# Optimization experiments

Measured on AMD Instinct MI355X. Metric: run time of the kernel, lower is better.

The kernel has to match this reference:

```python
import jax, jax.numpy as jnp
import numpy as np

B, S, D, H = 64, 2048, 64, 128  # batch, seq_len, input_dim, rnn_hidden_dim


def setup_inputs() -> dict:
    key = jax.random.key(0)
    k = jax.random.split(key, 6)
    x = jax.random.normal(k[0], (B, S, D), dtype=jnp.float32)
    # LSTM params, keras gate order: i, f, g(candidate), o
    Wx = jax.random.normal(k[1], (D, 4 * H), dtype=jnp.float32) / np.sqrt(D)
    Wh = jax.random.normal(k[2], (H, 4 * H), dtype=jnp.float32) / np.sqrt(H)
    b = jnp.zeros((4 * H,), dtype=jnp.float32).at[H:2 * H].set(1.0)  # unit_forget_bias
    # Dense(1, sigmoid) head
    Wd = jax.random.normal(k[3], (H, 1), dtype=jnp.float32) / np.sqrt(H)
    bd = jnp.zeros((1,), dtype=jnp.float32)
    return {"x": x, "Wx": Wx, "Wh": Wh, "b": b, "Wd": Wd, "bd": bd}


def _lstm_seq(x, Wx, Wh, b):
    H_ = Wh.shape[0]
    # precompute input projections for all timesteps: [B,S,4H]
    xz = jnp.einsum('bsd,dg->bsg', x, Wx) + b

    def step(carry, xz_t):
        h, c = carry
        z = xz_t + h @ Wh  # [B,4H]
        i = jax.nn.sigmoid(z[:, :H_])
        f = jax.nn.sigmoid(z[:, H_:2 * H_])
        g = jnp.tanh(z[:, 2 * H_:3 * H_])
        o = jax.nn.sigmoid(z[:, 3 * H_:])
        c = f * c + i * g
        h = o * jnp.tanh(c)
        return (h, c), h

    h0 = jnp.zeros((x.shape[0], H_), dtype=x.dtype)
    c0 = jnp.zeros((x.shape[0], H_), dtype=x.dtype)
    _, hs = jax.lax.scan(step, (h0, c0), jnp.swapaxes(xz, 0, 1))  # hs: [S,B,H]
    return jnp.swapaxes(hs, 0, 1)  # [B,S,H]


def reference(x, Wx, Wh, b, Wd, bd):
    h = _lstm_seq(x, Wx, Wh, b)                 # [B,S,H]
    return jax.nn.sigmoid(h @ Wd + bd)          # [B,S,1]
```

## Files before the change

### kernel.cpp

```cpp
#include <hip/hip_runtime.h>

#define B_ 64
#define S_ 2048
#define D_ 64
#define H_ 128
#define G_ 512
#define CH 16

typedef float f32x4 __attribute__((ext_vector_type(4)));
typedef short bf16x8 __attribute__((ext_vector_type(8)));

#define MFMA16(a, b, c) __builtin_amdgcn_mfma_f32_16x16x32_bf16((a), (b), (c), 0, 0, 0)
#define RCPF(x) __builtin_amdgcn_rcpf(x)
#define LOG2E 1.442695041f

#if __has_builtin(__builtin_amdgcn_exp2f)
#define EXP2(x) __builtin_amdgcn_exp2f(x)
#else
#define EXP2(x) exp2f(x)
#endif

#define STEP_SYNC() do {                                  \
    asm volatile("s_waitcnt lgkmcnt(0)" ::: "memory");    \
    __builtin_amdgcn_s_barrier();                         \
    asm volatile("" ::: "memory");                        \
} while (0)

__device__ __forceinline__ short f2bf(float f) {
    unsigned u = __builtin_bit_cast(unsigned, f);
    return (short)((u + 0x7FFFu + ((u >> 16) & 1u)) >> 16);
}
__device__ __forceinline__ float bflo(unsigned u) { return __builtin_bit_cast(float, u << 16); }
__device__ __forceinline__ float bfhi(unsigned u) { return __builtin_bit_cast(float, u & 0xFFFF0000u); }
__device__ __forceinline__ float sigm_f(float x) { return RCPF(1.0f + EXP2(x * -LOG2E)); }
__device__ __forceinline__ float tanh_f(float x) {
    return __builtin_fmaf(2.0f, RCPF(1.0f + EXP2(x * (-2.0f * LOG2E))), -1.0f);
}

__launch_bounds__(512, 2)
__global__ void lstm_fused(const float* __restrict__ x, const float* __restrict__ Wx,
                           const float* __restrict__ Wh, const float* __restrict__ bias,
                           const float* __restrict__ Wd, const float* __restrict__ bd,
                           float* __restrict__ out) {
    const int tid = threadIdx.x;
    const int lane = tid & 63;
    const int wid = tid >> 6;
    const int l15 = lane & 15;
    const int l4 = lane >> 4;
    const int bb = blockIdx.x;

    __shared__ alignas(16) short hist[CH][H_];
    __shared__ alignas(16) short xbf[CH][72];
    __shared__ alignas(16) float xzc[CH][G_];

    ((unsigned*)hist)[tid] = 0u;
    ((unsigned*)hist)[tid + 512] = 0u;

    const int col0 = wid * 16 + l15;

    bf16x8 bh[4][4];
#pragma unroll
    for (int ct = 0; ct < 4; ++ct) {
        const int col = ct * H_ + col0;
#pragma unroll
        for (int kt = 0; kt < 4; ++kt) {
            bf16x8 v;
#pragma unroll
            for (int e = 0; e < 8; ++e)
                v[e] = f2bf(Wh[(kt * 32 + l4 * 8 + e) * G_ + col]);
            bh[ct][kt] = v;
        }
    }
    bf16x8 bx[4][2];
#pragma unroll
    for (int ct = 0; ct < 4; ++ct) {
        const int col = ct * H_ + col0;
#pragma unroll
        for (int kt = 0; kt < 2; ++kt) {
            bf16x8 v;
#pragma unroll
            for (int e = 0; e < 8; ++e)
                v[e] = f2bf(Wx[(kt * 32 + l4 * 8 + e) * G_ + col]);
            bx[ct][kt] = v;
        }
    }

    float bvr[4];
#pragma unroll
    for (int ct = 0; ct < 4; ++ct) bvr[ct] = bias[ct * H_ + col0];
    const float wd0 = Wd[lane * 2 + 0];
    const float wd1 = Wd[lane * 2 + 1];
    const float bdv = bd[0];
    float c_reg = 0.0f;

    const float* xb = x + (size_t)bb * S_ * D_;
    float* ob = out + (size_t)bb * S_;

    float xp0 = xb[tid * 2 + 0];
    float xp1 = xb[tid * 2 + 1];

    f32x4 acc0 = {0.f, 0.f, 0.f, 0.f}, acc1 = acc0, acc2 = acc0, acc3 = acc0;

    for (int tc = 0; tc < S_; tc += CH) {
        xbf[tid >> 5][(tid & 31) * 2 + 0] = f2bf(xp0);
        xbf[tid >> 5][(tid & 31) * 2 + 1] = f2bf(xp1);
        __syncthreads();
        if (tc + CH < S_) {
            xp0 = xb[(tc + CH) * D_ + tid * 2 + 0];
            xp1 = xb[(tc + CH) * D_ + tid * 2 + 1];
        }
#pragma unroll
        for (int ct = 0; ct < 4; ++ct) {
            f32x4 cacc = {bvr[ct], bvr[ct], bvr[ct], bvr[ct]};
#pragma unroll
            for (int kt = 0; kt < 2; ++kt) {
                const bf16x8 a = *reinterpret_cast<const bf16x8*>(&xbf[l15][kt * 32 + l4 * 8]);
                cacc = MFMA16(a, bx[ct][kt], cacc);
            }
#pragma unroll
            for (int r = 0; r < 4; ++r)
                xzc[l4 * 4 + r][col0 * 4 + ct] = cacc[r];
        }
        if (tc > 0) {
#pragma unroll
            for (int s = 0; s < 2; ++s) {
                const int row = wid * 2 + s;
                const unsigned hp = *reinterpret_cast<const unsigned*>(&hist[row][lane * 2]);
                float p = bflo(hp) * wd0 + bfhi(hp) * wd1;
                p += __shfl_xor(p, 1);  p += __shfl_xor(p, 2);  p += __shfl_xor(p, 4);
                p += __shfl_xor(p, 8);  p += __shfl_xor(p, 16); p += __shfl_xor(p, 32);
                if (lane == 0) ob[tc - CH + row] = sigm_f(p + bdv);
            }
        }
        __syncthreads();

#pragma unroll
        for (int tm = 0; tm < CH; ++tm) {
            const int prev = (tm + CH - 1) & (CH - 1);
            const short* hsrc = hist[prev];
            const bf16x8 a0 = *reinterpret_cast<const bf16x8*>(&hsrc[ 0 + l4 * 8]);
            const bf16x8 a1 = *reinterpret_cast<const bf16x8*>(&hsrc[32 + l4 * 8]);
            const bf16x8 a2 = *reinterpret_cast<const bf16x8*>(&hsrc[64 + l4 * 8]);
            const bf16x8 a3 = *reinterpret_cast<const bf16x8*>(&hsrc[96 + l4 * 8]);
            const f32x4 xzq = *reinterpret_cast<const f32x4*>(&xzc[tm][col0 * 4]);

            acc0[0] = xzq[0];  acc1[0] = xzq[1];  acc2[0] = xzq[2];  acc3[0] = xzq[3];

            acc0 = MFMA16(a0, bh[0][0], acc0);
            acc1 = MFMA16(a0, bh[1][0], acc1);
            acc2 = MFMA16(a0, bh[2][0], acc2);
            acc3 = MFMA16(a0, bh[3][0], acc3);
            acc0 = MFMA16(a1, bh[0][1], acc0);
            acc1 = MFMA16(a1, bh[1][1], acc1);
            acc2 = MFMA16(a1, bh[2][1], acc2);
            acc3 = MFMA16(a1, bh[3][1], acc3);
            acc0 = MFMA16(a2, bh[0][2], acc0);
            acc1 = MFMA16(a2, bh[1][2], acc1);
            acc2 = MFMA16(a2, bh[2][2], acc2);
            acc3 = MFMA16(a2, bh[3][2], acc3);
            acc0 = MFMA16(a3, bh[0][3], acc0);
            acc1 = MFMA16(a3, bh[1][3], acc1);
            acc2 = MFMA16(a3, bh[2][3], acc2);
            acc3 = MFMA16(a3, bh[3][3], acc3);

            const float iv = sigm_f(acc0[0]);
            const float fv = sigm_f(acc1[0]);
            const float gv = tanh_f(acc2[0]);
            const float ov = sigm_f(acc3[0]);

            c_reg = __builtin_fmaf(fv, c_reg, iv * gv);
            const float hv = ov * tanh_f(c_reg);

            if (lane < 16) hist[tm][col0] = f2bf(hv);
            STEP_SYNC();
        }
    }

#pragma unroll
    for (int s = 0; s < 2; ++s) {
        const int row = wid * 2 + s;
        const unsigned hp = *reinterpret_cast<const unsigned*>(&hist[row][lane * 2]);
        float p = bflo(hp) * wd0 + bfhi(hp) * wd1;
        p += __shfl_xor(p, 1);  p += __shfl_xor(p, 2);  p += __shfl_xor(p, 4);
        p += __shfl_xor(p, 8);  p += __shfl_xor(p, 16); p += __shfl_xor(p, 32);
        if (lane == 0) ob[S_ - CH + row] = sigm_f(p + bdv);
    }
}

extern "C" void kernel_launch(void* const* d_in, const int* in_sizes, int n_in,
                              void* d_out, int out_size, void* d_ws, size_t ws_size,
                              hipStream_t stream) {
    const float* x  = (const float*)d_in[0];
    const float* Wx = (const float*)d_in[1];
    const float* Wh = (const float*)d_in[2];
    const float* b  = (const float*)d_in[3];
    const float* Wd = (const float*)d_in[4];
    const float* bd = (const float*)d_in[5];
    float* out = (float*)d_out;

    lstm_fused<<<B_, 512, 0, stream>>>(x, Wx, Wh, b, Wd, bd, out);
}
```

Measured before the change: 955.5 us.

## Double-buffer h/xz chunks and interleave input projection into recurrent steps

Double-buffers the hidden-state history and the precomputed input projections, so the next chunk's x load, bf16 conversion, input-projection MFMAs and the previous chunk's dense-head output are spread across individual timesteps of the current chunk. This removes the two per-chunk __syncthreads phases that stalled the serial recurrence. It also folds the -log2e (and -2log2e for the candidate gate) scaling into Wx, Wh and bias, which drops the multiplies in the gate activations. The trade-off is more LDS use, more conditional code inside the unrolled step loop and higher register pressure, and the scaling is applied before bf16 rounding.

```diff
diff --git a/kernel.cpp b/kernel.cpp
--- a/kernel.cpp
+++ b/kernel.cpp
@@ -6,6 +6,7 @@
 #define H_ 128
 #define G_ 512
 #define CH 16
+#define NCHUNK (S_ / CH)
 
 typedef float f32x4 __attribute__((ext_vector_type(4)));
 typedef short bf16x8 __attribute__((ext_vector_type(8)));
@@ -33,9 +34,6 @@
 __device__ __forceinline__ float bflo(unsigned u) { return __builtin_bit_cast(float, u << 16); }
 __device__ __forceinline__ float bfhi(unsigned u) { return __builtin_bit_cast(float, u & 0xFFFF0000u); }
 __device__ __forceinline__ float sigm_f(float x) { return RCPF(1.0f + EXP2(x * -LOG2E)); }
-__device__ __forceinline__ float tanh_f(float x) {
-    return __builtin_fmaf(2.0f, RCPF(1.0f + EXP2(x * (-2.0f * LOG2E))), -1.0f);
-}
 
 __launch_bounds__(512, 2)
 __global__ void lstm_fused(const float* __restrict__ x, const float* __restrict__ Wx,
@@ -49,45 +47,50 @@
     const int l4 = lane >> 4;
     const int bb = blockIdx.x;
 
-    __shared__ alignas(16) short hist[CH][H_];
+    __shared__ alignas(16) short hbuf[2][CH][H_];
     __shared__ alignas(16) short xbf[CH][72];
-    __shared__ alignas(16) float xzc[CH][G_];
-
-    ((unsigned*)hist)[tid] = 0u;
-    ((unsigned*)hist)[tid + 512] = 0u;
+    __shared__ alignas(16) float xzc[2][CH][G_];
+
+    {
+        unsigned* hz = (unsigned*)hbuf;
+        hz[tid] = 0u; hz[tid + 512] = 0u; hz[tid + 1024] = 0u; hz[tid + 1536] = 0u;
+    }
 
     const int col0 = wid * 16 + l15;
 
     bf16x8 bh[4][4];
 #pragma unroll
     for (int ct = 0; ct < 4; ++ct) {
+        const float msc = (ct == 2) ? (-2.0f * LOG2E) : (-LOG2E);
         const int col = ct * H_ + col0;
 #pragma unroll
         for (int kt = 0; kt < 4; ++kt) {
             bf16x8 v;
 #pragma unroll
             for (int e = 0; e < 8; ++e)
-                v[e] = f2bf(Wh[(kt * 32 + l4 * 8 + e) * G_ + col]);
+                v[e] = f2bf(Wh[(kt * 32 + l4 * 8 + e) * G_ + col] * msc);
             bh[ct][kt] = v;
         }
     }
     bf16x8 bx[4][2];
 #pragma unroll
     for (int ct = 0; ct < 4; ++ct) {
+        const float msc = (ct == 2) ? (-2.0f * LOG2E) : (-LOG2E);
         const int col = ct * H_ + col0;
 #pragma unroll
         for (int kt = 0; kt < 2; ++kt) {
             bf16x8 v;
 #pragma unroll
             for (int e = 0; e < 8; ++e)
-                v[e] = f2bf(Wx[(kt * 32 + l4 * 8 + e) * G_ + col]);
+                v[e] = f2bf(Wx[(kt * 32 + l4 * 8 + e) * G_ + col] * msc);
             bx[ct][kt] = v;
         }
     }
 
     float bvr[4];
 #pragma unroll
-    for (int ct = 0; ct < 4; ++ct) bvr[ct] = bias[ct * H_ + col0];
+    for (int ct = 0; ct < 4; ++ct)
+        bvr[ct] = bias[ct * H_ + col0] * ((ct == 2) ? (-2.0f * LOG2E) : (-LOG2E));
     const float wd0 = Wd[lane * 2 + 0];
     const float wd1 = Wd[lane * 2 + 1];
     const float bdv = bd[0];
@@ -96,53 +99,47 @@
     const float* xb = x + (size_t)bb * S_ * D_;
     float* ob = out + (size_t)bb * S_;
 
-    float xp0 = xb[tid * 2 + 0];
-    float xp1 = xb[tid * 2 + 1];
-
-    f32x4 acc0 = {0.f, 0.f, 0.f, 0.f}, acc1 = acc0, acc2 = acc0, acc3 = acc0;
-
-    for (int tc = 0; tc < S_; tc += CH) {
-        xbf[tid >> 5][(tid & 31) * 2 + 0] = f2bf(xp0);
-        xbf[tid >> 5][(tid & 31) * 2 + 1] = f2bf(xp1);
+    float xp0, xp1;
+
+    {
+        const float a0v = xb[tid * 2 + 0];
+        const float a1v = xb[tid * 2 + 1];
+        const unsigned pk = ((unsigned)(unsigned short)f2bf(a0v)) |
+                            (((unsigned)(unsigned short)f2bf(a1v)) << 16);
+        *reinterpret_cast<unsigned*>(&xbf[tid >> 5][(tid & 31) * 2]) = pk;
         __syncthreads();
-        if (tc + CH < S_) {
-            xp0 = xb[(tc + CH) * D_ + tid * 2 + 0];
-            xp1 = xb[(tc + CH) * D_ + tid * 2 + 1];
-        }
+        xp0 = xb[CH * D_ + tid * 2 + 0];
+        xp1 = xb[CH * D_ + tid * 2 + 1];
 #pragma unroll
         for (int ct = 0; ct < 4; ++ct) {
-            f32x4 cacc = {bvr[ct], bvr[ct], bvr[ct], bvr[ct]};
+            f32x4 cc = {bvr[ct], bvr[ct], bvr[ct], bvr[ct]};
 #pragma unroll
             for (int kt = 0; kt < 2; ++kt) {
                 const bf16x8 a = *reinterpret_cast<const bf16x8*>(&xbf[l15][kt * 32 + l4 * 8]);
-                cacc = MFMA16(a, bx[ct][kt], cacc);
+                cc = MFMA16(a, bx[ct][kt], cc);
             }
 #pragma unroll
             for (int r = 0; r < 4; ++r)
-                xzc[l4 * 4 + r][col0 * 4 + ct] = cacc[r];
-        }
-        if (tc > 0) {
-#pragma unroll
-            for (int s = 0; s < 2; ++s) {
-                const int row = wid * 2 + s;
-                const unsigned hp = *reinterpret_cast<const unsigned*>(&hist[row][lane * 2]);
-                float p = bflo(hp) * wd0 + bfhi(hp) * wd1;
-                p += __shfl_xor(p, 1);  p += __shfl_xor(p, 2);  p += __shfl_xor(p, 4);
-                p += __shfl_xor(p, 8);  p += __shfl_xor(p, 16); p += __shfl_xor(p, 32);
-                if (lane == 0) ob[tc - CH + row] = sigm_f(p + bdv);
-            }
+                xzc[0][l4 * 4 + r][col0 * 4 + ct] = cc[r];
         }
         __syncthreads();
+    }
+
+    f32x4 acc0 = {0.f, 0.f, 0.f, 0.f}, acc1 = acc0, acc2 = acc0, acc3 = acc0;
+    bf16x8 gf0, gf1;
+
+    for (int k = 0; k < NCHUNK; ++k) {
+        const int cur = k & 1, prv = cur ^ 1;
+        const bool notlast = (k < NCHUNK - 1);
 
 #pragma unroll
         for (int tm = 0; tm < CH; ++tm) {
-            const int prev = (tm + CH - 1) & (CH - 1);
-            const short* hsrc = hist[prev];
+            const short* hsrc = (tm == 0) ? hbuf[prv][CH - 1] : hbuf[cur][tm - 1];
             const bf16x8 a0 = *reinterpret_cast<const bf16x8*>(&hsrc[ 0 + l4 * 8]);
             const bf16x8 a1 = *reinterpret_cast<const bf16x8*>(&hsrc[32 + l4 * 8]);
             const bf16x8 a2 = *reinterpret_cast<const bf16x8*>(&hsrc[64 + l4 * 8]);
             const bf16x8 a3 = *reinterpret_cast<const bf16x8*>(&hsrc[96 + l4 * 8]);
-            const f32x4 xzq = *reinterpret_cast<const f32x4*>(&xzc[tm][col0 * 4]);
+            const f32x4 xzq = *reinterpret_cast<const f32x4*>(&xzc[cur][tm][col0 * 4]);
 
             acc0[0] = xzq[0];  acc1[0] = xzq[1];  acc2[0] = xzq[2];  acc3[0] = xzq[3];
 
@@ -163,15 +160,50 @@
             acc2 = MFMA16(a3, bh[2][3], acc2);
             acc3 = MFMA16(a3, bh[3][3], acc3);
 
-            const float iv = sigm_f(acc0[0]);
-            const float fv = sigm_f(acc1[0]);
-            const float gv = tanh_f(acc2[0]);
-            const float ov = sigm_f(acc3[0]);
+            const float iv = RCPF(1.0f + EXP2(acc0[0]));
+            const float fv = RCPF(1.0f + EXP2(acc1[0]));
+            const float gv = __builtin_fmaf(2.0f, RCPF(1.0f + EXP2(acc2[0])), -1.0f);
+            const float ov = RCPF(1.0f + EXP2(acc3[0]));
 
             c_reg = __builtin_fmaf(fv, c_reg, iv * gv);
-            const float hv = ov * tanh_f(c_reg);
-
-            if (lane < 16) hist[tm][col0] = f2bf(hv);
+            const float th = __builtin_fmaf(
+                2.0f, RCPF(1.0f + EXP2(c_reg * (-2.0f * LOG2E))), -1.0f);
+            const float hv = ov * th;
+
+            if (lane < 16) hbuf[cur][tm][col0] = f2bf(hv);
+
+            if (tm == 0 && notlast) {
+                const unsigned pk = ((unsigned)(unsigned short)f2bf(xp0)) |
+                                    (((unsigned)(unsigned short)f2bf(xp1)) << 16);
+                *reinterpret_cast<unsigned*>(&xbf[tid >> 5][(tid & 31) * 2]) = pk;
+                if (k < NCHUNK - 2) {
+                    xp0 = xb[(k + 2) * CH * D_ + tid * 2 + 0];
+                    xp1 = xb[(k + 2) * CH * D_ + tid * 2 + 1];
+                }
+            }
+            if (tm == 1 && notlast)
+                gf0 = *reinterpret_cast<const bf16x8*>(&xbf[l15][ 0 + l4 * 8]);
+            if (tm == 3 && notlast)
+                gf1 = *reinterpret_cast<const bf16x8*>(&xbf[l15][32 + l4 * 8]);
+            if ((tm == 4 || tm == 6 || tm == 8 || tm == 10) && notlast) {
+                const int ct = (tm - 4) >> 1;
+                f32x4 cc = {bvr[ct], bvr[ct], bvr[ct], bvr[ct]};
+                cc = MFMA16(gf0, bx[ct][0], cc);
+                cc = MFMA16(gf1, bx[ct][1], cc);
+#pragma unroll
+                for (int r = 0; r < 4; ++r)
+                    xzc[prv][l4 * 4 + r][col0 * 4 + ct] = cc[r];
+            }
+            if ((tm == 5 || tm == 13) && k > 0) {
+                const int row = wid * 2 + (tm == 13 ? 1 : 0);
+                const unsigned hp =
+                    *reinterpret_cast<const unsigned*>(&hbuf[prv][row][lane * 2]);
+                float p = bflo(hp) * wd0 + bfhi(hp) * wd1;
+                p += __shfl_xor(p, 1);  p += __shfl_xor(p, 2);  p += __shfl_xor(p, 4);
+                p += __shfl_xor(p, 8);  p += __shfl_xor(p, 16); p += __shfl_xor(p, 32);
+                if (lane == 0) ob[(k - 1) * CH + row] = sigm_f(p + bdv);
+            }
+
             STEP_SYNC();
         }
     }
@@ -179,7 +211,7 @@
 #pragma unroll
     for (int s = 0; s < 2; ++s) {
         const int row = wid * 2 + s;
-        const unsigned hp = *reinterpret_cast<const unsigned*>(&hist[row][lane * 2]);
+        const unsigned hp = *reinterpret_cast<const unsigned*>(&hbuf[1][row][lane * 2]);
         float p = bflo(hp) * wd0 + bfhi(hp) * wd1;
         p += __shfl_xor(p, 1);  p += __shfl_xor(p, 2);  p += __shfl_xor(p, 4);
         p += __shfl_xor(p, 8);  p += __shfl_xor(p, 16); p += __shfl_xor(p, 32);
```

Result: no change. 954.4 us (-0.1%).

## Replace recurrent MFMA with per-lane fp16 dot2 matvec and gate shuffles

Applied to the files above, without the earlier changes.

Each lane now owns one gate column and holds that column of Wh in registers as 64 packed fp16 pairs. It computes the recurrent matvec with v_dot2 instructions on a broadcast LDS read of h, instead of sixteen 16x16x32 MFMAs where only row 0 of the output is useful. The -log2e scale for the activations is folded into Wh, Wx and the bias, so sigmoid and tanh share one exp2/rcp form. The four gates are exchanged with xor shuffles. The hidden state is stored as fp16 instead of bf16. This aims to remove wasted MFMA work and latency on the serial critical path, at the cost of 64 extra weight registers per lane, dependent dot2 chains, and fp16 range and precision risk.

```diff
diff --git a/kernel.cpp b/kernel.cpp
--- a/kernel.cpp
+++ b/kernel.cpp
@@ -9,6 +9,8 @@
 
 typedef float f32x4 __attribute__((ext_vector_type(4)));
 typedef short bf16x8 __attribute__((ext_vector_type(8)));
+typedef short short2v __attribute__((ext_vector_type(2)));
+typedef _Float16 half2v __attribute__((ext_vector_type(2)));
 
 #define MFMA16(a, b, c) __builtin_amdgcn_mfma_f32_16x16x32_bf16((a), (b), (c), 0, 0, 0)
 #define RCPF(x) __builtin_amdgcn_rcpf(x)
@@ -20,6 +22,15 @@
 #define EXP2(x) exp2f(x)
 #endif
 
+#if __has_builtin(__builtin_amdgcn_fdot2)
+#define DOT2(a, b, c) __builtin_amdgcn_fdot2((a), (b), (c), false)
+#else
+__device__ __forceinline__ float DOT2(half2v a, half2v b, float c) {
+    return __builtin_fmaf((float)a[1], (float)b[1],
+           __builtin_fmaf((float)a[0], (float)b[0], c));
+}
+#endif
+
 #define STEP_SYNC() do {                                  \
     asm volatile("s_waitcnt lgkmcnt(0)" ::: "memory");    \
     __builtin_amdgcn_s_barrier();                         \
@@ -30,12 +41,13 @@
     unsigned u = __builtin_bit_cast(unsigned, f);
     return (short)((u + 0x7FFFu + ((u >> 16) & 1u)) >> 16);
 }
-__device__ __forceinline__ float bflo(unsigned u) { return __builtin_bit_cast(float, u << 16); }
-__device__ __forceinline__ float bfhi(unsigned u) { return __builtin_bit_cast(float, u & 0xFFFF0000u); }
+__device__ __forceinline__ short f2h(float f) {
+    return __builtin_bit_cast(short, (_Float16)f);
+}
+__device__ __forceinline__ float h2f(short s) {
+    return (float)__builtin_bit_cast(_Float16, s);
+}
 __device__ __forceinline__ float sigm_f(float x) { return RCPF(1.0f + EXP2(x * -LOG2E)); }
-__device__ __forceinline__ float tanh_f(float x) {
-    return __builtin_fmaf(2.0f, RCPF(1.0f + EXP2(x * (-2.0f * LOG2E))), -1.0f);
-}
 
 __launch_bounds__(512, 2)
 __global__ void lstm_fused(const float* __restrict__ x, const float* __restrict__ Wx,
@@ -49,6 +61,10 @@
     const int l4 = lane >> 4;
     const int bb = blockIdx.x;
 
+    const int q = lane & 3;
+    const int u = wid * 16 + (lane >> 2);
+    const int col = q * H_ + u;
+
     __shared__ alignas(16) short hist[CH][H_];
     __shared__ alignas(16) short xbf[CH][72];
     __shared__ alignas(16) float xzc[CH][G_];
@@ -56,38 +72,39 @@
     ((unsigned*)hist)[tid] = 0u;
     ((unsigned*)hist)[tid + 512] = 0u;
 
-    const int col0 = wid * 16 + l15;
-
-    bf16x8 bh[4][4];
+    const float msc = (q == 2) ? (-2.0f * LOG2E) : (-LOG2E);
+    const float a_c = (q == 2) ? 2.0f : 1.0f;
+    const float b_c = (q == 2) ? -1.0f : 0.0f;
+
+    half2v wh[64];
+#pragma unroll
+    for (int p = 0; p < 64; ++p) {
+        half2v v;
+        v[0] = (_Float16)(Wh[(2 * p + 0) * G_ + col] * msc);
+        v[1] = (_Float16)(Wh[(2 * p + 1) * G_ + col] * msc);
+        wh[p] = v;
+    }
+
+    bf16x8 bx[4][2];
 #pragma unroll
     for (int ct = 0; ct < 4; ++ct) {
-        const int col = ct * H_ + col0;
-#pragma unroll
-        for (int kt = 0; kt < 4; ++kt) {
-            bf16x8 v;
-#pragma unroll
-            for (int e = 0; e < 8; ++e)
-                v[e] = f2bf(Wh[(kt * 32 + l4 * 8 + e) * G_ + col]);
-            bh[ct][kt] = v;
-        }
-    }
-    bf16x8 bx[4][2];
-#pragma unroll
-    for (int ct = 0; ct < 4; ++ct) {
-        const int col = ct * H_ + col0;
+        const float ms = (ct == 2) ? (-2.0f * LOG2E) : (-LOG2E);
+        const int colm = ct * H_ + wid * 16 + l15;
 #pragma unroll
         for (int kt = 0; kt < 2; ++kt) {
             bf16x8 v;
 #pragma unroll
             for (int e = 0; e < 8; ++e)
-                v[e] = f2bf(Wx[(kt * 32 + l4 * 8 + e) * G_ + col]);
+                v[e] = f2bf(Wx[(kt * 32 + l4 * 8 + e) * G_ + colm] * ms);
             bx[ct][kt] = v;
         }
     }
-
     float bvr[4];
 #pragma unroll
-    for (int ct = 0; ct < 4; ++ct) bvr[ct] = bias[ct * H_ + col0];
+    for (int ct = 0; ct < 4; ++ct)
+        bvr[ct] = bias[ct * H_ + wid * 16 + l15] *
+                  ((ct == 2) ? (-2.0f * LOG2E) : (-LOG2E));
+
     const float wd0 = Wd[lane * 2 + 0];
     const float wd1 = Wd[lane * 2 + 1];
     const float bdv = bd[0];
@@ -99,7 +116,8 @@
     float xp0 = xb[tid * 2 + 0];
     float xp1 = xb[tid * 2 + 1];
 
-    f32x4 acc0 = {0.f, 0.f, 0.f, 0.f}, acc1 = acc0, acc2 = acc0, acc3 = acc0;
+    const bool sb0 = (q & 1) != 0;
+    const bool sb1 = (q & 2) != 0;
 
     for (int tc = 0; tc < S_; tc += CH) {
         xbf[tid >> 5][(tid & 31) * 2 + 0] = f2bf(xp0);
@@ -111,22 +129,22 @@
         }
 #pragma unroll
         for (int ct = 0; ct < 4; ++ct) {
-            f32x4 cacc = {bvr[ct], bvr[ct], bvr[ct], bvr[ct]};
+            f32x4 cc = {bvr[ct], bvr[ct], bvr[ct], bvr[ct]};
 #pragma unroll
             for (int kt = 0; kt < 2; ++kt) {
                 const bf16x8 a = *reinterpret_cast<const bf16x8*>(&xbf[l15][kt * 32 + l4 * 8]);
-                cacc = MFMA16(a, bx[ct][kt], cacc);
+                cc = MFMA16(a, bx[ct][kt], cc);
             }
 #pragma unroll
             for (int r = 0; r < 4; ++r)
-                xzc[l4 * 4 + r][col0 * 4 + ct] = cacc[r];
+                xzc[l4 * 4 + r][(wid * 16 + l15) * 4 + ct] = cc[r];
         }
         if (tc > 0) {
 #pragma unroll
             for (int s = 0; s < 2; ++s) {
                 const int row = wid * 2 + s;
-                const unsigned hp = *reinterpret_cast<const unsigned*>(&hist[row][lane * 2]);
-                float p = bflo(hp) * wd0 + bfhi(hp) * wd1;
+                const short2v hp = *reinterpret_cast<const short2v*>(&hist[row][lane * 2]);
+                float p = h2f(hp[0]) * wd0 + h2f(hp[1]) * wd1;
                 p += __shfl_xor(p, 1);  p += __shfl_xor(p, 2);  p += __shfl_xor(p, 4);
                 p += __shfl_xor(p, 8);  p += __shfl_xor(p, 16); p += __shfl_xor(p, 32);
                 if (lane == 0) ob[tc - CH + row] = sigm_f(p + bdv);
@@ -138,40 +156,37 @@
         for (int tm = 0; tm < CH; ++tm) {
             const int prev = (tm + CH - 1) & (CH - 1);
             const short* hsrc = hist[prev];
-            const bf16x8 a0 = *reinterpret_cast<const bf16x8*>(&hsrc[ 0 + l4 * 8]);
-            const bf16x8 a1 = *reinterpret_cast<const bf16x8*>(&hsrc[32 + l4 * 8]);
-            const bf16x8 a2 = *reinterpret_cast<const bf16x8*>(&hsrc[64 + l4 * 8]);
-            const bf16x8 a3 = *reinterpret_cast<const bf16x8*>(&hsrc[96 + l4 * 8]);
-            const f32x4 xzq = *reinterpret_cast<const f32x4*>(&xzc[tm][col0 * 4]);
-
-            acc0[0] = xzq[0];  acc1[0] = xzq[1];  acc2[0] = xzq[2];  acc3[0] = xzq[3];
-
-            acc0 = MFMA16(a0, bh[0][0], acc0);
-            acc1 = MFMA16(a0, bh[1][0], acc1);
-            acc2 = MFMA16(a0, bh[2][0], acc2);
-            acc3 = MFMA16(a0, bh[3][0], acc3);
-            acc0 = MFMA16(a1, bh[0][1], acc0);
-            acc1 = MFMA16(a1, bh[1][1], acc1);
-            acc2 = MFMA16(a1, bh[2][1], acc2);
-            acc3 = MFMA16(a1, bh[3][1], acc3);
-            acc0 = MFMA16(a2, bh[0][2], acc0);
-            acc1 = MFMA16(a2, bh[1][2], acc1);
-            acc2 = MFMA16(a2, bh[2][2], acc2);
-            acc3 = MFMA16(a2, bh[3][2], acc3);
-            acc0 = MFMA16(a3, bh[0][3], acc0);
-            acc1 = MFMA16(a3, bh[1][3], acc1);
-            acc2 = MFMA16(a3, bh[2][3], acc2);
-            acc3 = MFMA16(a3, bh[3][3], acc3);
-
-            const float iv = sigm_f(acc0[0]);
-            const float fv = sigm_f(acc1[0]);
-            const float gv = tanh_f(acc2[0]);
-            const float ov = sigm_f(acc3[0]);
-
-            c_reg = __builtin_fmaf(fv, c_reg, iv * gv);
-            const float hv = ov * tanh_f(c_reg);
-
-            if (lane < 16) hist[tm][col0] = f2bf(hv);
+
+            float za = xzc[tm][u * 4 + q], zb = 0.0f, zc2 = 0.0f, zd = 0.0f;
+#pragma unroll
+            for (int j = 0; j < 16; ++j) {
+                const bf16x8 hr = *reinterpret_cast<const bf16x8*>(&hsrc[j * 8]);
+                const short2v s0 = {hr[0], hr[1]};
+                const short2v s1 = {hr[2], hr[3]};
+                const short2v s2 = {hr[4], hr[5]};
+                const short2v s3 = {hr[6], hr[7]};
+                za  = DOT2(__builtin_bit_cast(half2v, s0), wh[j * 4 + 0], za);
+                zb  = DOT2(__builtin_bit_cast(half2v, s1), wh[j * 4 + 1], zb);
+                zc2 = DOT2(__builtin_bit_cast(half2v, s2), wh[j * 4 + 2], zc2);
+                zd  = DOT2(__builtin_bit_cast(half2v, s3), wh[j * 4 + 3], zd);
+            }
+            const float z = (za + zb) + (zc2 + zd);
+
+            const float t = __builtin_fmaf(a_c, RCPF(1.0f + EXP2(z)), b_c);
+
+            const float t1 = __shfl_xor(t, 1);
+            const float t2 = __shfl_xor(t, 2);
+            const float t3 = __shfl_xor(t, 3);
+            const float ig = sb0 ? (t1 * t3) : (t * t2);
+            const float fv = sb0 ? (sb1 ? t2 : t) : (sb1 ? t3 : t1);
+            const float ov = sb0 ? (sb1 ? t : t2) : (sb1 ? t1 : t3);
+
+            c_reg = __builtin_fmaf(fv, c_reg, ig);
+            const float th = __builtin_fmaf(
+                2.0f, RCPF(1.0f + EXP2(c_reg * (-2.0f * LOG2E))), -1.0f);
+            const float hv = ov * th;
+
+            if (q == 0) hist[tm][u] = f2h(hv);
             STEP_SYNC();
         }
     }
@@ -179,8 +194,8 @@
 #pragma unroll
     for (int s = 0; s < 2; ++s) {
         const int row = wid * 2 + s;
-        const unsigned hp = *reinterpret_cast<const unsigned*>(&hist[row][lane * 2]);
-        float p = bflo(hp) * wd0 + bfhi(hp) * wd1;
+        const short2v hp = *reinterpret_cast<const short2v*>(&hist[row][lane * 2]);
+        float p = h2f(hp[0]) * wd0 + h2f(hp[1]) * wd1;
         p += __shfl_xor(p, 1);  p += __shfl_xor(p, 2);  p += __shfl_xor(p, 4);
         p += __shfl_xor(p, 8);  p += __shfl_xor(p, 16); p += __shfl_xor(p, 32);
         if (lane == 0) ob[S_ - CH + row] = sigm_f(p + bdv);
```

Measured after the change: 1.298 ms. 1.36x slower.

## Halve LSTM block to 4 waves with two hidden tiles per wave, prescaled gates

Applied to the files above, without the earlier changes.

Cuts the block from 8 to 4 waves, so each wave computes 32 hidden units (8 accumulator tiles) per timestep. This halves the number of waves meeting at each per-step barrier. The input weights move from registers into an LDS transposed copy to make room for the doubled Wh register footprint. The weights and bias are prescaled by -log2e (or -2log2e for the candidate gate) so the gate activations skip a multiply. The cost is a longer serial MFMA chain per wave each step, plus LDS reads of Wx in the chunk projection.

```diff
diff --git a/kernel.cpp b/kernel.cpp
--- a/kernel.cpp
+++ b/kernel.cpp
@@ -6,6 +6,7 @@
 #define H_ 128
 #define G_ 512
 #define CH 16
+#define T_ 256
 
 typedef float f32x4 __attribute__((ext_vector_type(4)));
 typedef short bf16x8 __attribute__((ext_vector_type(8)));
@@ -33,11 +34,8 @@
 __device__ __forceinline__ float bflo(unsigned u) { return __builtin_bit_cast(float, u << 16); }
 __device__ __forceinline__ float bfhi(unsigned u) { return __builtin_bit_cast(float, u & 0xFFFF0000u); }
 __device__ __forceinline__ float sigm_f(float x) { return RCPF(1.0f + EXP2(x * -LOG2E)); }
-__device__ __forceinline__ float tanh_f(float x) {
-    return __builtin_fmaf(2.0f, RCPF(1.0f + EXP2(x * (-2.0f * LOG2E))), -1.0f);
-}
-
-__launch_bounds__(512, 2)
+
+__launch_bounds__(256, 1)
 __global__ void lstm_fused(const float* __restrict__ x, const float* __restrict__ Wx,
                            const float* __restrict__ Wh, const float* __restrict__ bias,
                            const float* __restrict__ Wd, const float* __restrict__ bd,
@@ -49,82 +47,94 @@
     const int l4 = lane >> 4;
     const int bb = blockIdx.x;
 
+    __shared__ alignas(16) short wxt[G_][72];
+    __shared__ alignas(16) float xzc[CH][G_];
     __shared__ alignas(16) short hist[CH][H_];
     __shared__ alignas(16) short xbf[CH][72];
-    __shared__ alignas(16) float xzc[CH][G_];
-
-    ((unsigned*)hist)[tid] = 0u;
-    ((unsigned*)hist)[tid + 512] = 0u;
-
-    const int col0 = wid * 16 + l15;
-
-    bf16x8 bh[4][4];
-#pragma unroll
-    for (int ct = 0; ct < 4; ++ct) {
-        const int col = ct * H_ + col0;
-#pragma unroll
-        for (int kt = 0; kt < 4; ++kt) {
-            bf16x8 v;
-#pragma unroll
-            for (int e = 0; e < 8; ++e)
-                v[e] = f2bf(Wh[(kt * 32 + l4 * 8 + e) * G_ + col]);
-            bh[ct][kt] = v;
-        }
-    }
-    bf16x8 bx[4][2];
-#pragma unroll
-    for (int ct = 0; ct < 4; ++ct) {
-        const int col = ct * H_ + col0;
-#pragma unroll
-        for (int kt = 0; kt < 2; ++kt) {
-            bf16x8 v;
-#pragma unroll
-            for (int e = 0; e < 8; ++e)
-                v[e] = f2bf(Wx[(kt * 32 + l4 * 8 + e) * G_ + col]);
-            bx[ct][kt] = v;
-        }
-    }
-
-    float bvr[4];
-#pragma unroll
-    for (int ct = 0; ct < 4; ++ct) bvr[ct] = bias[ct * H_ + col0];
+
+    {
+        unsigned* hz = (unsigned*)hist;
+        hz[tid] = 0u; hz[tid + 256] = 0u; hz[tid + 512] = 0u; hz[tid + 768] = 0u;
+    }
+    for (int i = tid; i < G_ * D_; i += T_) {
+        const int colx = i & (G_ - 1);
+        const int row = i >> 9;
+        const float ms = ((colx >> 7) == 2) ? (-2.0f * LOG2E) : (-LOG2E);
+        wxt[colx][row] = f2bf(Wx[i] * ms);
+    }
+
+    bf16x8 bh[8][4];
+    float bvr[8];
+#pragma unroll
+    for (int hh = 0; hh < 2; ++hh) {
+#pragma unroll
+        for (int g = 0; g < 4; ++g) {
+            const float msc = (g == 2) ? (-2.0f * LOG2E) : (-LOG2E);
+            const int col = g * H_ + wid * 32 + hh * 16 + l15;
+            bvr[hh * 4 + g] = bias[col] * msc;
+#pragma unroll
+            for (int kt = 0; kt < 4; ++kt) {
+                bf16x8 v;
+#pragma unroll
+                for (int e = 0; e < 8; ++e)
+                    v[e] = f2bf(Wh[(kt * 32 + l4 * 8 + e) * G_ + col] * msc);
+                bh[hh * 4 + g][kt] = v;
+            }
+        }
+    }
+
     const float wd0 = Wd[lane * 2 + 0];
     const float wd1 = Wd[lane * 2 + 1];
     const float bdv = bd[0];
-    float c_reg = 0.0f;
+    float cA = 0.0f, cB = 0.0f;
 
     const float* xb = x + (size_t)bb * S_ * D_;
     float* ob = out + (size_t)bb * S_;
 
-    float xp0 = xb[tid * 2 + 0];
-    float xp1 = xb[tid * 2 + 1];
-
-    f32x4 acc0 = {0.f, 0.f, 0.f, 0.f}, acc1 = acc0, acc2 = acc0, acc3 = acc0;
+    float xp0 = xb[tid * 4 + 0], xp1 = xb[tid * 4 + 1];
+    float xp2 = xb[tid * 4 + 2], xp3 = xb[tid * 4 + 3];
+
+    f32x4 acc[8];
+#pragma unroll
+    for (int j = 0; j < 8; ++j) acc[j] = (f32x4){0.f, 0.f, 0.f, 0.f};
 
     for (int tc = 0; tc < S_; tc += CH) {
-        xbf[tid >> 5][(tid & 31) * 2 + 0] = f2bf(xp0);
-        xbf[tid >> 5][(tid & 31) * 2 + 1] = f2bf(xp1);
+        {
+            short* xr = &xbf[tid >> 4][(tid & 15) * 4];
+            xr[0] = f2bf(xp0); xr[1] = f2bf(xp1); xr[2] = f2bf(xp2); xr[3] = f2bf(xp3);
+        }
         __syncthreads();
         if (tc + CH < S_) {
-            xp0 = xb[(tc + CH) * D_ + tid * 2 + 0];
-            xp1 = xb[(tc + CH) * D_ + tid * 2 + 1];
-        }
-#pragma unroll
-        for (int ct = 0; ct < 4; ++ct) {
-            f32x4 cacc = {bvr[ct], bvr[ct], bvr[ct], bvr[ct]};
-#pragma unroll
-            for (int kt = 0; kt < 2; ++kt) {
-                const bf16x8 a = *reinterpret_cast<const bf16x8*>(&xbf[l15][kt * 32 + l4 * 8]);
-                cacc = MFMA16(a, bx[ct][kt], cacc);
+            xp0 = xb[(tc + CH) * D_ + tid * 4 + 0];
+            xp1 = xb[(tc + CH) * D_ + tid * 4 + 1];
+            xp2 = xb[(tc + CH) * D_ + tid * 4 + 2];
+            xp3 = xb[(tc + CH) * D_ + tid * 4 + 3];
+        }
+#pragma unroll
+        for (int hh = 0; hh < 2; ++hh) {
+#pragma unroll
+            for (int g = 0; g < 4; ++g) {
+                const int col = g * H_ + wid * 32 + hh * 16 + l15;
+                const float bv = bvr[hh * 4 + g];
+                f32x4 cc = {bv, bv, bv, bv};
+#pragma unroll
+                for (int kt = 0; kt < 2; ++kt) {
+                    const bf16x8 a = *reinterpret_cast<const bf16x8*>(
+                        &xbf[l15][kt * 32 + l4 * 8]);
+                    const bf16x8 b = *reinterpret_cast<const bf16x8*>(
+                        &wxt[col][kt * 32 + l4 * 8]);
+                    cc = MFMA16(a, b, cc);
+                }
+                const int unit = wid * 32 + hh * 16 + l15;
+#pragma unroll
+                for (int r = 0; r < 4; ++r)
+                    xzc[l4 * 4 + r][unit * 4 + g] = cc[r];
             }
-#pragma unroll
-            for (int r = 0; r < 4; ++r)
-                xzc[l4 * 4 + r][col0 * 4 + ct] = cacc[r];
         }
         if (tc > 0) {
 #pragma unroll
-            for (int s = 0; s < 2; ++s) {
-                const int row = wid * 2 + s;
+            for (int s = 0; s < 4; ++s) {
+                const int row = wid * 4 + s;
                 const unsigned hp = *reinterpret_cast<const unsigned*>(&hist[row][lane * 2]);
                 float p = bflo(hp) * wd0 + bfhi(hp) * wd1;
                 p += __shfl_xor(p, 1);  p += __shfl_xor(p, 2);  p += __shfl_xor(p, 4);
@@ -142,43 +152,51 @@
             const bf16x8 a1 = *reinterpret_cast<const bf16x8*>(&hsrc[32 + l4 * 8]);
             const bf16x8 a2 = *reinterpret_cast<const bf16x8*>(&hsrc[64 + l4 * 8]);
             const bf16x8 a3 = *reinterpret_cast<const bf16x8*>(&hsrc[96 + l4 * 8]);
-            const f32x4 xzq = *reinterpret_cast<const f32x4*>(&xzc[tm][col0 * 4]);
-
-            acc0[0] = xzq[0];  acc1[0] = xzq[1];  acc2[0] = xzq[2];  acc3[0] = xzq[3];
-
-            acc0 = MFMA16(a0, bh[0][0], acc0);
-            acc1 = MFMA16(a0, bh[1][0], acc1);
-            acc2 = MFMA16(a0, bh[2][0], acc2);
-            acc3 = MFMA16(a0, bh[3][0], acc3);
-            acc0 = MFMA16(a1, bh[0][1], acc0);
-            acc1 = MFMA16(a1, bh[1][1], acc1);
-            acc2 = MFMA16(a1, bh[2][1], acc2);
-            acc3 = MFMA16(a1, bh[3][1], acc3);
-            acc0 = MFMA16(a2, bh[0][2], acc0);
-            acc1 = MFMA16(a2, bh[1][2], acc1);
-            acc2 = MFMA16(a2, bh[2][2], acc2);
-            acc3 = MFMA16(a2, bh[3][2], acc3);
-            acc0 = MFMA16(a3, bh[0][3], acc0);
-            acc1 = MFMA16(a3, bh[1][3], acc1);
-            acc2 = MFMA16(a3, bh[2][3], acc2);
-            acc3 = MFMA16(a3, bh[3][3], acc3);
-
-            const float iv = sigm_f(acc0[0]);
-            const float fv = sigm_f(acc1[0]);
-            const float gv = tanh_f(acc2[0]);
-            const float ov = sigm_f(acc3[0]);
-
-            c_reg = __builtin_fmaf(fv, c_reg, iv * gv);
-            const float hv = ov * tanh_f(c_reg);
-
-            if (lane < 16) hist[tm][col0] = f2bf(hv);
+            const int uA = wid * 32 + l15;
+            const f32x4 xzA = *reinterpret_cast<const f32x4*>(&xzc[tm][uA * 4]);
+            const f32x4 xzB = *reinterpret_cast<const f32x4*>(&xzc[tm][(uA + 16) * 4]);
+
+            acc[0][0] = xzA[0];  acc[1][0] = xzA[1];
+            acc[2][0] = xzA[2];  acc[3][0] = xzA[3];
+            acc[4][0] = xzB[0];  acc[5][0] = xzB[1];
+            acc[6][0] = xzB[2];  acc[7][0] = xzB[3];
+
+#pragma unroll
+            for (int j = 0; j < 8; ++j) acc[j] = MFMA16(a0, bh[j][0], acc[j]);
+#pragma unroll
+            for (int j = 0; j < 8; ++j) acc[j] = MFMA16(a1, bh[j][1], acc[j]);
+#pragma unroll
+            for (int j = 0; j < 8; ++j) acc[j] = MFMA16(a2, bh[j][2], acc[j]);
+#pragma unroll
+            for (int j = 0; j < 8; ++j) acc[j] = MFMA16(a3, bh[j][3], acc[j]);
+
+            const float ivA = RCPF(1.0f + EXP2(acc[0][0]));
+            const float fvA = RCPF(1.0f + EXP2(acc[1][0]));
+            const float gvA = __builtin_fmaf(2.0f, RCPF(1.0f + EXP2(acc[2][0])), -1.0f);
+            const float ovA = RCPF(1.0f + EXP2(acc[3][0]));
+            cA = __builtin_fmaf(fvA, cA, ivA * gvA);
+            const float thA = __builtin_fmaf(
+                2.0f, RCPF(1.0f + EXP2(cA * (-2.0f * LOG2E))), -1.0f);
+            const float hvA = ovA * thA;
+
+            const float ivB = RCPF(1.0f + EXP2(acc[4][0]));
+            const float fvB = RCPF(1.0f + EXP2(acc[5][0]));
+            const float gvB = __builtin_fmaf(2.0f, RCPF(1.0f + EXP2(acc[6][0])), -1.0f);
+            const float ovB = RCPF(1.0f + EXP2(acc[7][0]));
+            cB = __builtin_fmaf(fvB, cB, ivB * gvB);
+            const float thB = __builtin_fmaf(
+                2.0f, RCPF(1.0f + EXP2(cB * (-2.0f * LOG2E))), -1.0f);
+            const float hvB = ovB * thB;
+
+            if (l4 == 0)      hist[tm][uA]      = f2bf(hvA);
+            else if (l4 == 1) hist[tm][uA + 16] = f2bf(hvB);
             STEP_SYNC();
         }
     }
 
 #pragma unroll
-    for (int s = 0; s < 2; ++s) {
-        const int row = wid * 2 + s;
+    for (int s = 0; s < 4; ++s) {
+        const int row = wid * 4 + s;
         const unsigned hp = *reinterpret_cast<const unsigned*>(&hist[row][lane * 2]);
         float p = bflo(hp) * wd0 + bfhi(hp) * wd1;
         p += __shfl_xor(p, 1);  p += __shfl_xor(p, 2);  p += __shfl_xor(p, 4);
@@ -198,5 +216,5 @@
     const float* bd = (const float*)d_in[5];
     float* out = (float*)d_out;
 
-    lstm_fused<<<B_, 512, 0, stream>>>(x, Wx, Wh, b, Wd, bd, out);
+    lstm_fused<<<B_, T_, 0, stream>>>(x, Wx, Wh, b, Wd, bd, out);
 }
```

Result: slower. 1.333 ms (+39.5%).
